# Kernel optimization log

Measured on AMD Instinct MI355X. Metric: run time of the kernel, lower is better.

## Reference

```python
import jax, jax.numpy as jnp
import numpy as np

N_NODES = 100000
N_EDGES = 400000
IN_DIM = 100
OUT_DIM = 200
NUM_STEPS = 4


def setup_inputs() -> dict:
    key = jax.random.key(0)
    ks = jax.random.split(key, 8)
    x = jax.random.normal(ks[0], (N_NODES, IN_DIM), dtype=jnp.float32)
    edge_index = jax.random.randint(ks[1], (2, N_EDGES), 0, N_NODES, dtype=jnp.int64)
    s = 0.05
    W = jax.random.normal(ks[2], (NUM_STEPS, OUT_DIM, OUT_DIM), dtype=jnp.float32) * s
    w_ih = jax.random.normal(ks[3], (3 * OUT_DIM, OUT_DIM), dtype=jnp.float32) * s
    w_hh = jax.random.normal(ks[4], (3 * OUT_DIM, OUT_DIM), dtype=jnp.float32) * s
    b_ih = jax.random.normal(ks[5], (3 * OUT_DIM,), dtype=jnp.float32) * s
    b_hh = jax.random.normal(ks[6], (3 * OUT_DIM,), dtype=jnp.float32) * s
    cls_w = jax.random.normal(ks[7], (2, OUT_DIM), dtype=jnp.float32) * s
    cls_b = jnp.zeros((2,), dtype=jnp.float32)
    return {"x": x, "W": W, "w_ih": w_ih, "w_hh": w_hh, "b_ih": b_ih,
            "b_hh": b_hh, "cls_w": cls_w, "cls_b": cls_b, "edge_index": edge_index}


def _gru_cell(a, h, w_ih, w_hh, b_ih, b_hh):
    # torch.nn.GRUCell math: input a, hidden h
    gi = a @ w_ih.T + b_ih          # [N, 3D]
    gh = h @ w_hh.T + b_hh          # [N, 3D]
    i_r, i_z, i_n = jnp.split(gi, 3, axis=1)
    h_r, h_z, h_n = jnp.split(gh, 3, axis=1)
    r = jax.nn.sigmoid(i_r + h_r)
    z = jax.nn.sigmoid(i_z + h_z)
    n = jnp.tanh(i_n + r * h_n)
    return (1.0 - z) * n + z * h


def reference(x, W, w_ih, w_hh, b_ih, b_hh, cls_w, cls_b, edge_index):
    N = x.shape[0]
    # GatedGraphConv pads input features with zeros up to out_channels
    h = jnp.pad(x, ((0, 0), (0, OUT_DIM - x.shape[1])))
    src, dst = edge_index[0], edge_index[1]
    for i in range(NUM_STEPS):
        m = h @ W[i]                                         # [N, D]
        aggr = jax.ops.segment_sum(m[src], dst, num_segments=N)  # scatter-add
        h = _gru_cell(aggr, h, w_ih, w_hh, b_ih, b_hh)
    out = jax.nn.relu(h)
    # global_max_pool with all-zero batch ids -> max over all nodes
    pooled = jnp.max(out, axis=0, keepdims=True)             # [1, D]
    logits = pooled @ cls_w.T + cls_b                        # [1, 2]
    return jax.nn.softmax(logits, axis=1)
```

## Files before the change

kernel.cpp:

```cpp
#include <hip/hip_runtime.h>
#include <hip/hip_bf16.h>
#include <math.h>

#define N_NODES 100000
#define N_PAD   100096
#define N_EDGES 400000
#define IN_DIM  100
#define D       200
#define DP      208
#define KP      224
#define NUM_STEPS 4

#define TILE_SHORTS  21504
#define HALF_SHORTS  10752
#define HALF_GROUPS  21
#define EIDX_CAP     896

typedef __attribute__((ext_vector_type(8))) short bfrag;
typedef __attribute__((ext_vector_type(4))) float facc;

__device__ short g_Wall[NUM_STEPS * 13 * TILE_SHORTS];
__device__ float g_bias[6 * DP];

__device__ __forceinline__ float fast_sigmoid(float x) {
    return __builtin_amdgcn_rcpf(1.0f + __expf(-x));
}
__device__ __forceinline__ float fast_tanh(float x) {
    return 2.0f * __builtin_amdgcn_rcpf(1.0f + __expf(-2.0f * x)) - 1.0f;
}
__device__ __forceinline__ float bf2f(short u) {
    unsigned int x = ((unsigned int)(unsigned short)u) << 16;
    return __uint_as_float(x);
}

__global__ __launch_bounds__(256) void wconv_kernel(const float* __restrict__ W,
                                                    const float* __restrict__ w_ih,
                                                    const float* __restrict__ w_hh,
                                                    const float* __restrict__ b_ih,
                                                    const float* __restrict__ b_hh) {
    if (blockIdx.x >= 546) {
        int idx = (blockIdx.x - 546) * 256 + threadIdx.x;
        if (idx < 6 * DP) {
            int g = idx / DP, j = idx % DP;
            float v = 0.0f;
            if (j < D) v = (g < 3) ? b_ih[g * 200 + j] : b_hh[(g - 3) * 200 + j];
            g_bias[idx] = v;
        }
        return;
    }
    int idx = blockIdx.x * 256 + threadIdx.x;
    int l  = idx & 63;
    int t  = (idx >> 6) % 7;
    int g  = (idx / 448) % 6;
    int jt = (idx / 2688) % 13;
    int s  = idx / 34944;
    int j  = jt * 16 + (l & 15);
    int k0 = t * 32 + (l >> 4) * 8;
    short* out = g_Wall + (size_t)idx * 8;
    float vals[8];
    if (g < 3) {
        const float* wr = (j < D) ? &w_ih[(size_t)(g * 200 + j) * D] : nullptr;
        #pragma unroll
        for (int i = 0; i < 8; ++i) vals[i] = 0.0f;
        if (wr) {
            #pragma unroll
            for (int i = 0; i < 8; ++i) {
                int k = k0 + i;
                if (k < D) {
                    const float* Wr = &W[(size_t)s * D * D + (size_t)k * D];
                    float acc = 0.0f;
                    #pragma unroll 4
                    for (int tt = 0; tt < D; ++tt) acc += wr[tt] * Wr[tt];
                    vals[i] = acc;
                }
            }
        }
    } else {
        #pragma unroll
        for (int i = 0; i < 8; ++i) {
            int k = k0 + i;
            vals[i] = (j < D && k < D) ? w_hh[((size_t)(g - 3) * 200 + j) * D + k] : 0.0f;
        }
    }
    #pragma unroll
    for (int i = 0; i < 8; ++i) {
        __hip_bfloat16 b = __float2bfloat16(vals[i]);
        out[i] = *reinterpret_cast<short*>(&b);
    }
}

__global__ void pad_kernel(const float* __restrict__ x, __hip_bfloat16* __restrict__ h) {
    int idx = blockIdx.x * 256 + threadIdx.x;
    int n = idx / KP, c = idx % KP;
    float v = (n < N_NODES && c < IN_DIM) ? x[n * IN_DIM + c] : 0.0f;
    h[idx] = __float2bfloat16(v);
}

__global__ void count_kernel(const int* __restrict__ dst, int* __restrict__ cnt) {
    int e = blockIdx.x * blockDim.x + threadIdx.x;
    if (e < N_EDGES) atomicAdd(&cnt[dst[e]], 1);
}

#define SCAN_B 1024
#define NB_SCAN ((N_NODES + SCAN_B - 1) / SCAN_B)
__global__ __launch_bounds__(SCAN_B) void scan1(const int* __restrict__ cnt,
                                                int* __restrict__ incl, int* __restrict__ bsum) {
    __shared__ int ws[16];
    int i = blockIdx.x * SCAN_B + threadIdx.x;
    int lane = threadIdx.x & 63, wid = threadIdx.x >> 6;
    int v = (i < N_NODES) ? cnt[i] : 0;
    int s = v;
    #pragma unroll
    for (int o = 1; o < 64; o <<= 1) {
        int t = __shfl_up(s, o, 64);
        if (lane >= o) s += t;
    }
    if (lane == 63) ws[wid] = s;
    __syncthreads();
    if (wid == 0) {
        int t = (lane < 16) ? ws[lane] : 0;
        #pragma unroll
        for (int o = 1; o < 16; o <<= 1) {
            int u = __shfl_up(t, o, 64);
            if (lane >= o) t += u;
        }
        if (lane < 16) ws[lane] = t;
    }
    __syncthreads();
    if (wid > 0) s += ws[wid - 1];
    if (i < N_NODES) incl[i] = s;
    if (threadIdx.x == SCAN_B - 1) bsum[blockIdx.x] = s;
}
__global__ void scan3(const int* __restrict__ cnt, const int* __restrict__ incl,
                      const int* __restrict__ bsum, int* __restrict__ off,
                      int* __restrict__ cursor) {
    __shared__ int sh[128];
    if (threadIdx.x < 128) sh[threadIdx.x] = (threadIdx.x < NB_SCAN) ? bsum[threadIdx.x] : 0;
    __syncthreads();
    for (int o = 1; o < 128; o <<= 1) {
        int t = (threadIdx.x >= o && threadIdx.x < 128) ? sh[threadIdx.x - o] : 0;
        __syncthreads();
        if (threadIdx.x < 128) sh[threadIdx.x] += t;
        __syncthreads();
    }
    int i = blockIdx.x * blockDim.x + threadIdx.x;
    if (i < N_NODES) {
        int b = i / SCAN_B;
        int pre = b ? sh[b - 1] : 0;
        int v = incl[i] - cnt[i] + pre;
        off[i] = v; cursor[i] = v;
    }
    if (i == 0) off[N_NODES] = N_EDGES;
}
__global__ void fill_kernel(const int* __restrict__ src, const int* __restrict__ dst,
                            int* __restrict__ cursor, int* __restrict__ esrc) {
    int e = blockIdx.x * blockDim.x + threadIdx.x;
    if (e < N_EDGES) {
        int pos = atomicAdd(&cursor[dst[e]], 1);
        esrc[pos] = src[e];
    }
}

__device__ __forceinline__ void stage_half(const short* __restrict__ gsrc,
                                           short* lds_dst, int wave, int lane) {
    #pragma unroll
    for (int g = wave; g < HALF_GROUPS; g += 4) {
        __builtin_amdgcn_global_load_lds(
            (const __attribute__((address_space(1))) void*)(gsrc + g * 512 + lane * 8),
            (__attribute__((address_space(3))) void*)(lds_dst + g * 512),
            16, 0, 0);
    }
}

__global__ __launch_bounds__(256, 2) void gru_fused(const __hip_bfloat16* __restrict__ hcur,
                                                    __hip_bfloat16* __restrict__ hnext,
                                                    const int* __restrict__ off,
                                                    const int* __restrict__ esrc,
                                                    unsigned int* __restrict__ pooled,
                                                    int step) {
    __shared__ short Bs[2][HALF_SHORTS];
    __shared__ unsigned int pmax[DP];
    int tid = threadIdx.x;
    int lane = tid & 63, wave = tid >> 6;
    int wbase = blockIdx.x * 128 + wave * 32;
    int mrow = lane & 15, kq = lane >> 4;
    bool dopool = (step == NUM_STEPS - 1);

    if (dopool) for (int c = tid; c < DP; c += 256) pmax[c] = 0u;

    short* LDSbase = &Bs[0][0];
    short* Awave = LDSbase + wave * 16 * KP;
    int* EIdx = (int*)((char*)LDSbase + 28672) + wave * EIDX_CAP;

    int nlo = wbase < N_NODES ? wbase : N_NODES;
    int nhi = (wbase + 32) < N_NODES ? (wbase + 32) : N_NODES;
    int lo = off[nlo];
    int cntw = off[nhi] - lo;
    bool use_lds = (cntw <= EIDX_CAP);
    if (use_lds)
        for (int i = lane; i < cntw; i += 64) EIdx[i] = esrc[lo + i];

    bfrag av[2][7], hv[2][7];

    int r4 = lane >> 4;
    int ck = lane & 15;
    int colA = ck * 8;
    int colB = colA + 128;
    bool sumB = (ck < 9);
    #pragma unroll
    for (int p = 0; p < 2; ++p) {
        #pragma unroll
        for (int it = 0; it < 4; ++it) {
            int rr = it * 4 + r4;
            int n = wbase + p * 16 + rr;
            float a[8] = {0, 0, 0, 0, 0, 0, 0, 0};
            float b[8] = {0, 0, 0, 0, 0, 0, 0, 0};
            if (n < N_NODES) {
                int e0 = off[n] - lo, e1 = off[n + 1] - lo;
                int e = e0;
                for (; e + 3 < e1; e += 4) {
                    int i0, i1, i2, i3;
                    if (use_lds) {
                        i0 = EIdx[e]; i1 = EIdx[e + 1]; i2 = EIdx[e + 2]; i3 = EIdx[e + 3];
                    } else {
                        i0 = esrc[lo + e];     i1 = esrc[lo + e + 1];
                        i2 = esrc[lo + e + 2]; i3 = esrc[lo + e + 3];
                    }
                    size_t s0 = (size_t)i0 * KP, s1 = (size_t)i1 * KP;
                    size_t s2 = (size_t)i2 * KP, s3 = (size_t)i3 * KP;
                    bfrag a0 = *(const bfrag*)(hcur + s0 + colA);
                    bfrag a1 = *(const bfrag*)(hcur + s1 + colA);
                    bfrag a2 = *(const bfrag*)(hcur + s2 + colA);
                    bfrag a3 = *(const bfrag*)(hcur + s3 + colA);
                    if (sumB) {
                        bfrag b0 = *(const bfrag*)(hcur + s0 + colB);
                        bfrag b1 = *(const bfrag*)(hcur + s1 + colB);
                        bfrag b2 = *(const bfrag*)(hcur + s2 + colB);
                        bfrag b3 = *(const bfrag*)(hcur + s3 + colB);
                        #pragma unroll
                        for (int q = 0; q < 8; ++q)
                            b[q] += (bf2f(b0[q]) + bf2f(b1[q])) + (bf2f(b2[q]) + bf2f(b3[q]));
                    }
                    #pragma unroll
                    for (int q = 0; q < 8; ++q)
                        a[q] += (bf2f(a0[q]) + bf2f(a1[q])) + (bf2f(a2[q]) + bf2f(a3[q]));
                }
                for (; e < e1; ++e) {
                    int i0 = use_lds ? EIdx[e] : esrc[lo + e];
                    size_t s0 = (size_t)i0 * KP;
                    bfrag a0 = *(const bfrag*)(hcur + s0 + colA);
                    if (sumB) {
                        bfrag b0 = *(const bfrag*)(hcur + s0 + colB);
                        #pragma unroll
                        for (int q = 0; q < 8; ++q) b[q] += bf2f(b0[q]);
                    }
                    #pragma unroll
                    for (int q = 0; q < 8; ++q) a[q] += bf2f(a0[q]);
                }
            }
            __hip_bfloat16 oa[8], ob[8];
            #pragma unroll
            for (int q = 0; q < 8; ++q) {
                oa[q] = __float2bfloat16(a[q]);
                ob[q] = __float2bfloat16(b[q]);
            }
            *(ushort4*)(Awave + rr * KP + colA)     = *(const ushort4*)&oa[0];
            *(ushort4*)(Awave + rr * KP + colA + 4) = *(const ushort4*)&oa[4];
            if (ck < 12) {
                *(ushort4*)(Awave + rr * KP + colB)     = *(const ushort4*)&ob[0];
                *(ushort4*)(Awave + rr * KP + colB + 4) = *(const ushort4*)&ob[4];
            }
        }
        #pragma unroll
        for (int t = 0; t < 7; ++t)
            av[p][t] = *(const bfrag*)&Awave[mrow * KP + t * 32 + kq * 8];
    }

    size_t hbase = (size_t)(wbase + mrow) * KP + kq * 8;
    #pragma unroll
    for (int mf = 0; mf < 2; ++mf)
        #pragma unroll
        for (int t = 0; t < 7; ++t)
            hv[mf][t] = *(const bfrag*)(hcur + hbase + mf * 16 * KP + t * 32);

    const short* Wstep = g_Wall + (size_t)step * 13 * TILE_SHORTS;
    int jcol = lane & 15;
    int rowq = (lane >> 4) * 4;

    __syncthreads();
    stage_half(Wstep, &Bs[0][0], wave, lane);

    facc acc[6][2];
    unsigned short hold_u[2][4];

    for (int hk = 0; hk < 26; ++hk) {
        __syncthreads();
        if (hk + 1 < 26)
            stage_half(Wstep + (size_t)(hk + 1) * HALF_SHORTS,
                       &Bs[(hk + 1) & 1][0], wave, lane);

        int jt = hk >> 1;
        int j = jt * 16 + jcol;
        const short* Bcur = &Bs[hk & 1][0];

        if ((hk & 1) == 0) {
            #pragma unroll
            for (int mf = 0; mf < 2; ++mf)
                #pragma unroll
                for (int r = 0; r < 4; ++r)
                    hold_u[mf][r] = *(const unsigned short*)
                        (hcur + (size_t)(wbase + mf * 16 + rowq + r) * KP + j);
            #pragma unroll
            for (int g = 0; g < 6; ++g)
                #pragma unroll
                for (int mf = 0; mf < 2; ++mf) acc[g][mf] = (facc)(0.0f);
            #pragma unroll
            for (int t = 0; t < 7; ++t) {
                bfrag bv[3];
                #pragma unroll
                for (int g = 0; g < 3; ++g)
                    bv[g] = *(const bfrag*)&Bcur[(size_t)(((g * 7 + t) * 64) + lane) * 8];
                #pragma unroll
                for (int g = 0; g < 3; ++g)
                    #pragma unroll
                    for (int mf = 0; mf < 2; ++mf)
                        acc[g][mf] = __builtin_amdgcn_mfma_f32_16x16x32_bf16(av[mf][t], bv[g], acc[g][mf], 0, 0, 0);
            }
        } else {
            #pragma unroll
            for (int t = 0; t < 7; ++t) {
                bfrag bv[3];
                #pragma unroll
                for (int g = 0; g < 3; ++g)
                    bv[g] = *(const bfrag*)&Bcur[(size_t)(((g * 7 + t) * 64) + lane) * 8];
                #pragma unroll
                for (int g = 0; g < 3; ++g)
                    #pragma unroll
                    for (int mf = 0; mf < 2; ++mf)
                        acc[g + 3][mf] = __builtin_amdgcn_mfma_f32_16x16x32_bf16(hv[mf][t], bv[g], acc[g + 3][mf], 0, 0, 0);
            }

            float tmax = 0.0f;
            if (j < D) {
                float bir = g_bias[j],          biz = g_bias[DP + j],     bin = g_bias[2 * DP + j];
                float bhr = g_bias[3 * DP + j], bhz = g_bias[4 * DP + j], bhn = g_bias[5 * DP + j];
                #pragma unroll
                for (int mf = 0; mf < 2; ++mf) {
                    int m0 = wbase + mf * 16 + rowq;
                    #pragma unroll
                    for (int r = 0; r < 4; ++r) {
                        int m = m0 + r;
                        if (m < N_NODES) {
                            float hold = bf2f((short)hold_u[mf][r]);
                            float rr = fast_sigmoid(acc[0][mf][r] + bir + acc[3][mf][r] + bhr);
                            float zz = fast_sigmoid(acc[1][mf][r] + biz + acc[4][mf][r] + bhz);
                            float nn = fast_tanh(acc[2][mf][r] + bin + rr * (acc[5][mf][r] + bhn));
                            float hv2 = (1.0f - zz) * nn + zz * hold;
                            hnext[(size_t)m * KP + j] = __float2bfloat16(hv2);
                            if (hv2 > tmax) tmax = hv2;
                        }
                    }
                }
                if (dopool) atomicMax(&pmax[j], __float_as_uint(tmax));
            }
        }
    }

    if (dopool) {
        __syncthreads();
        for (int c = tid; c < D; c += 256) atomicMax(&pooled[c], pmax[c]);
    }
}

__global__ void head_kernel(const unsigned int* __restrict__ pooled,
                            const float* __restrict__ cls_w,
                            const float* __restrict__ cls_b,
                            float* __restrict__ out) {
    if (threadIdx.x == 0) {
        float l0 = cls_b[0], l1 = cls_b[1];
        for (int d = 0; d < D; ++d) {
            float p = __uint_as_float(pooled[d]);
            l0 += p * cls_w[d];
            l1 += p * cls_w[D + d];
        }
        float mx = l0 > l1 ? l0 : l1;
        float e0 = expf(l0 - mx), e1 = expf(l1 - mx);
        out[0] = e0 / (e0 + e1);
        out[1] = e1 / (e0 + e1);
    }
}

extern "C" void kernel_launch(void* const* d_in, const int* in_sizes, int n_in,
                              void* d_out, int out_size, void* d_ws, size_t ws_size,
                              hipStream_t stream) {
    const float* x     = (const float*)d_in[0];
    const float* W     = (const float*)d_in[1];
    const float* w_ih  = (const float*)d_in[2];
    const float* w_hh  = (const float*)d_in[3];
    const float* b_ih  = (const float*)d_in[4];
    const float* b_hh  = (const float*)d_in[5];
    const float* cls_w = (const float*)d_in[6];
    const float* cls_b = (const float*)d_in[7];
    const int*   ei    = (const int*)d_in[8];
    const int* src = ei;
    const int* dst = ei + N_EDGES;

    const size_t ROWB = (size_t)N_PAD * KP;
    __hip_bfloat16* hA   = (__hip_bfloat16*)d_ws;
    __hip_bfloat16* hB   = hA + ROWB;
    int* cnt    = (int*)(hB + ROWB);
    int* incl   = cnt + N_NODES;
    int* bsum   = incl + N_NODES;
    int* off    = bsum + 128;
    int* cursor = off + N_NODES + 1;
    int* esrc   = cursor + N_NODES;
    unsigned int* pooled = (unsigned int*)(esrc + N_EDGES);

    hipMemsetAsync(cnt, 0, N_NODES * sizeof(int), stream);
    count_kernel<<<(N_EDGES + 255) / 256, 256, 0, stream>>>(dst, cnt);
    scan1<<<NB_SCAN, SCAN_B, 0, stream>>>(cnt, incl, bsum);
    scan3<<<(N_NODES + 255) / 256, 256, 0, stream>>>(cnt, incl, bsum, off, cursor);
    fill_kernel<<<(N_EDGES + 255) / 256, 256, 0, stream>>>(src, dst, cursor, esrc);

    wconv_kernel<<<551, 256, 0, stream>>>(W, w_ih, w_hh, b_ih, b_hh);

    pad_kernel<<<(int)(ROWB / 256), 256, 0, stream>>>(x, hA);
    hipMemsetAsync(pooled, 0, D * sizeof(unsigned int), stream);

    __hip_bfloat16* hcur = hA;
    __hip_bfloat16* hnext = hB;
    for (int s = 0; s < NUM_STEPS; ++s) {
        gru_fused<<<N_PAD / 128, 256, 0, stream>>>(hcur, hnext, off, esrc, pooled, s);
        __hip_bfloat16* t = hcur; hcur = hnext; hnext = t;
    }
    head_kernel<<<1, 64, 0, stream>>>(pooled, cls_w, cls_b, (float*)d_out);
}
```

Before: 833.0 us.

## Compact weight tiles in LDS and drop h register cache to raise occupancy

Repacks the precomputed weight tiles so that the last K-chunk (k 192-199) is stored only for the lanes that carry data, which shrinks each staged half-tile in LDS and the EIdx buffer. It stops caching the full hidden-state fragments in registers and loads them per K-step from global memory. Launch bounds go from 2 to 4 blocks per SM, the aim being more resident waves to hide gather latency. The neighbour gathers also become nontemporal loads. In exchange there are extra global loads of h, branchy zero-padding of fragments, and possible spilling under the tighter register budget.

```diff
diff --git a/kernel.cpp b/kernel.cpp
--- a/kernel.cpp
+++ b/kernel.cpp
@@ -11,15 +11,16 @@
 #define KP      224
 #define NUM_STEPS 4
 
-#define TILE_SHORTS  21504
-#define HALF_SHORTS  10752
-#define HALF_GROUPS  21
-#define EIDX_CAP     896
+#define HALF_SHORTS   9728
+#define STAGE_GROUPS  19
+#define EIDX_CAP      608
+#define WCHUNKS_PER_SJT 2432
+#define WCONV_BLOCKS  494
 
 typedef __attribute__((ext_vector_type(8))) short bfrag;
 typedef __attribute__((ext_vector_type(4))) float facc;
 
-__device__ short g_Wall[NUM_STEPS * 13 * TILE_SHORTS];
+__device__ short g_Wall[NUM_STEPS * 13 * 2 * HALF_SHORTS];
 __device__ float g_bias[6 * DP];
 
 __device__ __forceinline__ float fast_sigmoid(float x) {
@@ -38,8 +39,8 @@
                                                     const float* __restrict__ w_hh,
                                                     const float* __restrict__ b_ih,
                                                     const float* __restrict__ b_hh) {
-    if (blockIdx.x >= 546) {
-        int idx = (blockIdx.x - 546) * 256 + threadIdx.x;
+    if (blockIdx.x >= WCONV_BLOCKS) {
+        int idx = (blockIdx.x - WCONV_BLOCKS) * 256 + threadIdx.x;
         if (idx < 6 * DP) {
             int g = idx / DP, j = idx % DP;
             float v = 0.0f;
@@ -49,14 +50,24 @@
         return;
     }
     int idx = blockIdx.x * 256 + threadIdx.x;
-    int l  = idx & 63;
-    int t  = (idx >> 6) % 7;
-    int g  = (idx / 448) % 6;
-    int jt = (idx / 2688) % 13;
-    int s  = idx / 34944;
+    short* out = g_Wall + (size_t)idx * 8;
+    int s    = idx / (13 * WCHUNKS_PER_SJT);
+    int rem  = idx % (13 * WCHUNKS_PER_SJT);
+    int jt   = rem / WCHUNKS_PER_SJT;
+    int r2   = rem % WCHUNKS_PER_SJT;
+    int half = r2 / 1216;
+    int c    = r2 % 1216;
+    if (c >= 1200) {
+        #pragma unroll
+        for (int i = 0; i < 8; ++i) out[i] = 0;
+        return;
+    }
+    int gg = c / 400, cc = c % 400;
+    int t  = (cc < 384) ? (cc >> 6) : 6;
+    int l  = (cc < 384) ? (cc & 63) : (cc - 384);
+    int g  = half * 3 + gg;
     int j  = jt * 16 + (l & 15);
     int k0 = t * 32 + (l >> 4) * 8;
-    short* out = g_Wall + (size_t)idx * 8;
     float vals[8];
     if (g < 3) {
         const float* wr = (j < D) ? &w_ih[(size_t)(g * 200 + j) * D] : nullptr;
@@ -164,7 +175,7 @@
 __device__ __forceinline__ void stage_half(const short* __restrict__ gsrc,
                                            short* lds_dst, int wave, int lane) {
     #pragma unroll
-    for (int g = wave; g < HALF_GROUPS; g += 4) {
+    for (int g = wave; g < STAGE_GROUPS; g += 4) {
         __builtin_amdgcn_global_load_lds(
             (const __attribute__((address_space(1))) void*)(gsrc + g * 512 + lane * 8),
             (__attribute__((address_space(3))) void*)(lds_dst + g * 512),
@@ -172,13 +183,22 @@
     }
 }
 
-__global__ __launch_bounds__(256, 2) void gru_fused(const __hip_bfloat16* __restrict__ hcur,
+__device__ __forceinline__ bfrag bv_load(const short* Bcur, int g, int t, int lane) {
+    if (t < 6) return *(const bfrag*)(Bcur + g * 3200 + t * 512 + lane * 8);
+    bfrag z;
+    #pragma unroll
+    for (int i = 0; i < 8; ++i) z[i] = 0;
+    if (lane < 16) z = *(const bfrag*)(Bcur + g * 3200 + 3072 + lane * 8);
+    return z;
+}
+
+__global__ __launch_bounds__(256, 4) void gru_fused(const __hip_bfloat16* __restrict__ hcur,
                                                     __hip_bfloat16* __restrict__ hnext,
                                                     const int* __restrict__ off,
                                                     const int* __restrict__ esrc,
                                                     unsigned int* __restrict__ pooled,
                                                     int step) {
-    __shared__ short Bs[2][HALF_SHORTS];
+    __shared__ __align__(16) short Bs[2][HALF_SHORTS];
     __shared__ unsigned int pmax[DP];
     int tid = threadIdx.x;
     int lane = tid & 63, wave = tid >> 6;
@@ -200,7 +220,7 @@
     if (use_lds)
         for (int i = lane; i < cntw; i += 64) EIdx[i] = esrc[lo + i];
 
-    bfrag av[2][7], hv[2][7];
+    bfrag av[2][7];
 
     int r4 = lane >> 4;
     int ck = lane & 15;
@@ -228,15 +248,15 @@
                     }
                     size_t s0 = (size_t)i0 * KP, s1 = (size_t)i1 * KP;
                     size_t s2 = (size_t)i2 * KP, s3 = (size_t)i3 * KP;
-                    bfrag a0 = *(const bfrag*)(hcur + s0 + colA);
-                    bfrag a1 = *(const bfrag*)(hcur + s1 + colA);
-                    bfrag a2 = *(const bfrag*)(hcur + s2 + colA);
-                    bfrag a3 = *(const bfrag*)(hcur + s3 + colA);
+                    bfrag a0 = __builtin_nontemporal_load((const bfrag*)(hcur + s0 + colA));
+                    bfrag a1 = __builtin_nontemporal_load((const bfrag*)(hcur + s1 + colA));
+                    bfrag a2 = __builtin_nontemporal_load((const bfrag*)(hcur + s2 + colA));
+                    bfrag a3 = __builtin_nontemporal_load((const bfrag*)(hcur + s3 + colA));
                     if (sumB) {
-                        bfrag b0 = *(const bfrag*)(hcur + s0 + colB);
-                        bfrag b1 = *(const bfrag*)(hcur + s1 + colB);
-                        bfrag b2 = *(const bfrag*)(hcur + s2 + colB);
-                        bfrag b3 = *(const bfrag*)(hcur + s3 + colB);
+                        bfrag b0 = __builtin_nontemporal_load((const bfrag*)(hcur + s0 + colB));
+                        bfrag b1 = __builtin_nontemporal_load((const bfrag*)(hcur + s1 + colB));
+                        bfrag b2 = __builtin_nontemporal_load((const bfrag*)(hcur + s2 + colB));
+                        bfrag b3 = __builtin_nontemporal_load((const bfrag*)(hcur + s3 + colB));
                         #pragma unroll
                         for (int q = 0; q < 8; ++q)
                             b[q] += (bf2f(b0[q]) + bf2f(b1[q])) + (bf2f(b2[q]) + bf2f(b3[q]));
@@ -248,9 +268,9 @@
                 for (; e < e1; ++e) {
                     int i0 = use_lds ? EIdx[e] : esrc[lo + e];
                     size_t s0 = (size_t)i0 * KP;
-                    bfrag a0 = *(const bfrag*)(hcur + s0 + colA);
+                    bfrag a0 = __builtin_nontemporal_load((const bfrag*)(hcur + s0 + colA));
                     if (sumB) {
-                        bfrag b0 = *(const bfrag*)(hcur + s0 + colB);
+                        bfrag b0 = __builtin_nontemporal_load((const bfrag*)(hcur + s0 + colB));
                         #pragma unroll
                         for (int q = 0; q < 8; ++q) b[q] += bf2f(b0[q]);
                     }
@@ -276,16 +296,11 @@
             av[p][t] = *(const bfrag*)&Awave[mrow * KP + t * 32 + kq * 8];
     }
 
-    size_t hbase = (size_t)(wbase + mrow) * KP + kq * 8;
-    #pragma unroll
-    for (int mf = 0; mf < 2; ++mf)
-        #pragma unroll
-        for (int t = 0; t < 7; ++t)
-            hv[mf][t] = *(const bfrag*)(hcur + hbase + mf * 16 * KP + t * 32);
-
-    const short* Wstep = g_Wall + (size_t)step * 13 * TILE_SHORTS;
+    const short* Wstep = g_Wall + (size_t)step * 13 * (2 * HALF_SHORTS);
     int jcol = lane & 15;
     int rowq = (lane >> 4) * 4;
+    const __hip_bfloat16* hrow0 = hcur + (size_t)(wbase + mrow) * KP;
+    const __hip_bfloat16* hrow1 = hrow0 + (size_t)16 * KP;
 
     __syncthreads();
     stage_half(Wstep, &Bs[0][0], wave, lane);
@@ -318,8 +333,7 @@
             for (int t = 0; t < 7; ++t) {
                 bfrag bv[3];
                 #pragma unroll
-                for (int g = 0; g < 3; ++g)
-                    bv[g] = *(const bfrag*)&Bcur[(size_t)(((g * 7 + t) * 64) + lane) * 8];
+                for (int g = 0; g < 3; ++g) bv[g] = bv_load(Bcur, g, t, lane);
                 #pragma unroll
                 for (int g = 0; g < 3; ++g)
                     #pragma unroll
@@ -329,15 +343,26 @@
         } else {
             #pragma unroll
             for (int t = 0; t < 7; ++t) {
+                bfrag h0, h1;
+                if (t < 6) {
+                    h0 = *(const bfrag*)(hrow0 + t * 32 + kq * 8);
+                    h1 = *(const bfrag*)(hrow1 + t * 32 + kq * 8);
+                } else {
+                    #pragma unroll
+                    for (int i = 0; i < 8; ++i) { h0[i] = 0; h1[i] = 0; }
+                    if (kq == 0) {
+                        h0 = *(const bfrag*)(hrow0 + 192);
+                        h1 = *(const bfrag*)(hrow1 + 192);
+                    }
+                }
                 bfrag bv[3];
                 #pragma unroll
-                for (int g = 0; g < 3; ++g)
-                    bv[g] = *(const bfrag*)&Bcur[(size_t)(((g * 7 + t) * 64) + lane) * 8];
-                #pragma unroll
-                for (int g = 0; g < 3; ++g)
-                    #pragma unroll
-                    for (int mf = 0; mf < 2; ++mf)
-                        acc[g + 3][mf] = __builtin_amdgcn_mfma_f32_16x16x32_bf16(hv[mf][t], bv[g], acc[g + 3][mf], 0, 0, 0);
+                for (int g = 0; g < 3; ++g) bv[g] = bv_load(Bcur, g, t, lane);
+                #pragma unroll
+                for (int g = 0; g < 3; ++g) {
+                    acc[g + 3][0] = __builtin_amdgcn_mfma_f32_16x16x32_bf16(h0, bv[g], acc[g + 3][0], 0, 0, 0);
+                    acc[g + 3][1] = __builtin_amdgcn_mfma_f32_16x16x32_bf16(h1, bv[g], acc[g + 3][1], 0, 0, 0);
+                }
             }
 
             float tmax = 0.0f;
@@ -422,7 +447,7 @@
     scan3<<<(N_NODES + 255) / 256, 256, 0, stream>>>(cnt, incl, bsum, off, cursor);
     fill_kernel<<<(N_EDGES + 255) / 256, 256, 0, stream>>>(src, dst, cursor, esrc);
 
-    wconv_kernel<<<551, 256, 0, stream>>>(W, w_ih, w_hh, b_ih, b_hh);
+    wconv_kernel<<<WCONV_BLOCKS + 5, 256, 0, stream>>>(W, w_ih, w_hh, b_ih, b_hh);
 
     pad_kernel<<<(int)(ROWB / 256), 256, 0, stream>>>(x, hA);
     hipMemsetAsync(pooled, 0, D * sizeof(unsigned int), stream);
```

Measured after the change: 1.478 ms. 77.4% more time.
